# Kernel tuning notes

Measured on AMD Instinct MI355X. Metric: run time of the kernel, lower is better.

Reference implementation:

```python
import jax, jax.numpy as jnp
import numpy as np

# Static configuration (matches init_kwargs / input_specs)
NUM_SEQS = 8          # sequences in the batch
H = 32                # query heads
H_KV = 8              # kv heads (GQA group = 4)
D = 128               # head dim
MEM_BLK = 64          # paged-cache block size (tokens per cache block)
CTX = 2048            # cached context length per sequence (uniform)
Q = 64                # new (diffusion-block) tokens per sequence
MAX_BLKS = CTX // MEM_BLK   # 32 blocks per sequence in block_tables
N_BLOCKS = 512        # total cache blocks in the pool
SCALE = 1.0 / float(np.sqrt(D))


def setup_inputs() -> dict:
    key = jax.random.key(0)
    k0, k1, k2, k3, k4 = jax.random.split(key, 5)
    T = NUM_SEQS * Q  # total new tokens (flat ragged layout)
    q = jax.random.normal(k0, (T, H, D), dtype=jnp.float32)
    k = jax.random.normal(k1, (T, H_KV, D), dtype=jnp.float32)
    v = jax.random.normal(k2, (T, H_KV, D), dtype=jnp.float32)
    k_cache = jax.random.normal(k3, (N_BLOCKS, MEM_BLK, H_KV, D), dtype=jnp.float32)
    v_cache = jax.random.normal(k4, (N_BLOCKS, MEM_BLK, H_KV, D), dtype=jnp.float32)
    # sequence s owns cache blocks [s*MAX_BLKS, (s+1)*MAX_BLKS)
    block_tables = jnp.arange(NUM_SEQS * MAX_BLKS, dtype=jnp.int32).reshape(NUM_SEQS, MAX_BLKS)
    # new tokens are written into freshly allocated slots beyond the context blocks
    slot_mapping = NUM_SEQS * MAX_BLKS * MEM_BLK + jnp.arange(T, dtype=jnp.int32)
    return {"q": q, "k": k, "v": v, "k_cache": k_cache, "v_cache": v_cache,
            "block_tables": block_tables, "slot_mapping": slot_mapping}


def reference(q, k, v, k_cache, v_cache, block_tables, slot_mapping):
    # --- store_kvcache: scatter new k/v rows into flat cache slots ---
    kc_flat = k_cache.reshape(-1, H_KV, D).at[slot_mapping].set(k)
    vc_flat = v_cache.reshape(-1, H_KV, D).at[slot_mapping].set(v)
    kc = kc_flat.reshape(N_BLOCKS, MEM_BLK, H_KV, D)
    vc = vc_flat.reshape(N_BLOCKS, MEM_BLK, H_KV, D)

    # --- load_kvcache: block-table indexed gather of context, concat new kv ---
    # ctx_k/ctx_v: [S, CTX, H_KV, D]
    ctx_k = kc[block_tables].reshape(NUM_SEQS, MAX_BLKS * MEM_BLK, H_KV, D)[:, :CTX]
    ctx_v = vc[block_tables].reshape(NUM_SEQS, MAX_BLKS * MEM_BLK, H_KV, D)[:, :CTX]
    k_new = k.reshape(NUM_SEQS, Q, H_KV, D)
    v_new = v.reshape(NUM_SEQS, Q, H_KV, D)
    k_full = jnp.concatenate([ctx_k, k_new], axis=1)  # [S, CTX+Q, H_KV, D]
    v_full = jnp.concatenate([ctx_v, v_new], axis=1)

    # --- flex attention with GQA: diffusion block attends to full context +
    #     bidirectionally within its own new block ---
    G = H // H_KV
    qg = q.reshape(NUM_SEQS, Q, H_KV, G, D)
    # scores: [S, H_KV, G, Q, CTX+Q]
    scores = jnp.einsum("sqhgd,skhd->shgqk", qg, k_full) * SCALE
    attn = jax.nn.softmax(scores, axis=-1)
    out = jnp.einsum("shgqk,skhd->sqhgd", attn, v_full)  # [S, Q, H_KV, G, D]
    return out.reshape(NUM_SEQS * Q, H, D)
```

## Files before the change

### kernel.cpp

```cpp
#include <hip/hip_runtime.h>
#include <hip/hip_bf16.h>


typedef float  f32x16 __attribute__((ext_vector_type(16)));
typedef short  bf16x8 __attribute__((ext_vector_type(8)));

__device__ __forceinline__ unsigned pkbf(float lo, float hi) {
    union { __hip_bfloat162 h; unsigned u; } t;
    t.h.x = __float2bfloat16(lo);
    t.h.y = __float2bfloat16(hi);
    return t.u;
}

#define LWS_OFF (4u * 64u * 256u * 128u)

__launch_bounds__(512, 2)
__global__ void attn_part(const float* __restrict__ qg,
                          const float* __restrict__ kin,
                          const float* __restrict__ vin,
                          const float* __restrict__ kcache,
                          const float* __restrict__ vcache,
                          const int*   __restrict__ bt,
                          float* __restrict__ Ows,
                          float* __restrict__ Lws)
{
    __shared__ __align__(16) unsigned char smem[49152];

    const int bid   = blockIdx.x;
    const int grp   = bid & 63;
    const int slice = bid >> 6;
    const int s     = grp >> 3;
    const int hkv   = grp & 7;

    const int tid  = threadIdx.x;
    const int w    = tid >> 6;
    const int lane = tid & 63;
    const int l32  = lane & 31;
    const int hi2  = lane >> 5;
    const int g    = w >> 1;
    const int qh   = w & 1;

    unsigned char* KB = smem;
    unsigned char* VB = smem + 16384;
    unsigned char* PB = smem + 32768 + w * 2048;

    const float QSCALE = 0.08838834764831845f * 1.44269504088896340736f;

    bf16x8 aq[8];
    {
        const float* qp =
            qg + (size_t)((s * 64 + qh * 32 + l32) * 32 + hkv * 4 + g) * 128;
#pragma unroll
        for (int dc = 0; dc < 8; ++dc) {
            const float* p = qp + dc * 16 + hi2 * 8;
            const float4 f0 = *(const float4*)(p);
            const float4 f1 = *(const float4*)(p + 4);
            uint4 tt = make_uint4(pkbf(f0.x * QSCALE, f0.y * QSCALE),
                                  pkbf(f0.z * QSCALE, f0.w * QSCALE),
                                  pkbf(f1.x * QSCALE, f1.y * QSCALE),
                                  pkbf(f1.z * QSCALE, f1.w * QSCALE));
            aq[dc] = __builtin_bit_cast(bf16x8, tt);
        }
    }

    f32x16 acco[4];
#pragma unroll
    for (int dc = 0; dc < 4; ++dc) acco[dc] = (f32x16)0.f;
    float lsum = 0.f;

    const int vd  = tid & 127;
    const int vkg = tid >> 7;

    float4 kreg[2];
    float  vreg[8];

    const int tile0 = (slice < 2) ? slice * 17 : 34 + (slice - 2) * 16;
    const int nt    = (slice < 2) ? 17 : 16;

    auto load_regs = [&](int T) {
        const float *ks, *vs;
        if (T < 64) {
            const int blk = bt[s * 32 + (T >> 1)];
            const size_t base = (size_t)blk * 65536 + (size_t)(T & 1) * 32768 + hkv * 128;
            ks = kcache + base; vs = vcache + base;
        } else {
            const size_t base = (size_t)(s * 64 + (T & 1) * 32) * 1024 + hkv * 128;
            ks = kin + base; vs = vin + base;
        }
#pragma unroll
        for (int i = 0; i < 2; ++i) {
            const int f = tid + 512 * i;
            kreg[i] = *(const float4*)(ks + (size_t)(f >> 5) * 1024 + (f & 31) * 4);
        }
#pragma unroll
        for (int j = 0; j < 8; ++j)
            vreg[j] = vs[(size_t)(vkg * 8 + j) * 1024 + vd];
    };

    auto write_lds = [&](int buf) {
        unsigned char* K = KB + buf * 8192;
        unsigned char* V = VB + buf * 8192;
#pragma unroll
        for (int i = 0; i < 2; ++i) {
            const int f  = tid + 512 * i;
            const int kv = f >> 5;
            const int dk = f & 31;
            const int Xs = dk ^ ((kv & 15) << 1);
            *(uint2*)(K + kv * 256 + Xs * 8) =
                make_uint2(pkbf(kreg[i].x, kreg[i].y), pkbf(kreg[i].z, kreg[i].w));
        }
        const int u = vkg ^ ((vd >> 1) & 3);
        *(uint4*)(V + vd * 64 + u * 16) =
            make_uint4(pkbf(vreg[0], vreg[1]), pkbf(vreg[2], vreg[3]),
                       pkbf(vreg[4], vreg[5]), pkbf(vreg[6], vreg[7]));
    };

    const int vq = (l32 >> 1) & 3;

    auto compute = [&](int buf) {
        const unsigned char* K = KB + buf * 8192;
        const unsigned char* V = VB + buf * 8192;

        f32x16 sc = (f32x16)0.f;
#pragma unroll
        for (int dc = 0; dc < 8; ++dc) {
            const int u = (dc * 2 + hi2) ^ (l32 & 15);
            const bf16x8 ak = *(const bf16x8*)(K + l32 * 256 + u * 16);
            sc = __builtin_amdgcn_mfma_f32_32x32x16_bf16(ak, aq[dc], sc, 0, 0, 0);
        }

        float p[16];
#pragma unroll
        for (int r = 0; r < 16; ++r) {
            p[r] = __builtin_amdgcn_exp2f(sc[r]);
            lsum += p[r];
        }

#pragma unroll
        for (int rq = 0; rq < 4; ++rq)
#pragma unroll
            for (int e = 0; e < 2; ++e)
                *(unsigned*)(PB + l32 * 64 + ((rq ^ vq) * 16) + (2 * hi2 + e) * 4) =
                    pkbf(p[rq * 4 + 2 * e], p[rq * 4 + 2 * e + 1]);
        asm volatile("s_waitcnt lgkmcnt(0)" ::: "memory");

        bf16x8 pa[2];
#pragma unroll
        for (int kk = 0; kk < 2; ++kk)
            pa[kk] = *(const bf16x8*)(PB + l32 * 64 + (((kk * 2 + hi2) ^ vq) * 16));

#pragma unroll
        for (int kk = 0; kk < 2; ++kk)
#pragma unroll
            for (int d2 = 0; d2 < 4; ++d2) {
                const int u = (kk * 2 + hi2) ^ vq;
                const bf16x8 bv = *(const bf16x8*)(V + (d2 * 32 + l32) * 64 + u * 16);
                acco[d2] = __builtin_amdgcn_mfma_f32_32x32x16_bf16(pa[kk], bv, acco[d2], 0, 0, 0);
            }
    };

    load_regs(tile0);
    write_lds(0);
    load_regs(tile0 + 1);

    for (int tt = 0; tt < nt; ++tt) {
        __syncthreads();
        if (tt + 1 < nt) write_lds((tt + 1) & 1);
        if (tt + 2 < nt) load_regs(tile0 + tt + 2);
        compute(tt & 1);
    }

    const float lt = lsum + __shfl_xor(lsum, 32);
    const size_t gq = (size_t)(slice * 64 + grp) * 256 + w * 32;
    if (hi2 == 0) Lws[gq + l32] = lt;
    float* Od = Ows + gq * 128;
#pragma unroll
    for (int dc = 0; dc < 4; ++dc)
#pragma unroll
        for (int r = 0; r < 16; ++r) {
            const int qiw = (r & 3) + 8 * (r >> 2) + 4 * hi2;
            Od[(size_t)qiw * 128 + dc * 32 + l32] = acco[dc][r];
        }
}

__launch_bounds__(256)
__global__ void attn_combine(const float* __restrict__ Ows,
                             const float* __restrict__ Lws,
                             float* __restrict__ out)
{
    const int idx = blockIdx.x * 256 + threadIdx.x;
    const int dq  = idx & 31;
    const int qr  = (idx >> 5) & 255;
    const int grp = idx >> 13;
    const int s = grp >> 3, hkv = grp & 7;
    const int g = qr >> 6, qtok = qr & 63;

    float4 acc = make_float4(0.f, 0.f, 0.f, 0.f);
    float  l   = 0.f;
#pragma unroll
    for (int sl = 0; sl < 4; ++sl) {
        const size_t base = (size_t)(sl * 64 + grp) * 256 + qr;
        const float4 p = *(const float4*)(Ows + base * 128 + dq * 4);
        acc.x += p.x; acc.y += p.y; acc.z += p.z; acc.w += p.w;
        l += Lws[base];
    }
    const float inv = 1.0f / l;
    float4 o = make_float4(acc.x * inv, acc.y * inv, acc.z * inv, acc.w * inv);
    *(float4*)(out + ((size_t)((s * 64 + qtok) * 32 + hkv * 4 + g)) * 128 + dq * 4) = o;
}

extern "C" void kernel_launch(void* const* d_in, const int* in_sizes, int n_in,
                              void* d_out, int out_size, void* d_ws, size_t ws_size,
                              hipStream_t stream)
{
    const float* q  = (const float*)d_in[0];
    const float* k  = (const float*)d_in[1];
    const float* v  = (const float*)d_in[2];
    const float* kc = (const float*)d_in[3];
    const float* vc = (const float*)d_in[4];
    const int*   bt = (const int*)d_in[5];
    float* Ows = (float*)d_ws;
    float* Lws = Ows + LWS_OFF;
    float* o   = (float*)d_out;

    attn_part<<<dim3(256), dim3(512), 0, stream>>>(q, k, v, kc, vc, bt, Ows, Lws);
    attn_combine<<<dim3(2048), dim3(256), 0, stream>>>(Ows, Lws, o);
}
```

Before: 45.79 us.

## Split each block's KV tiles across two wave halves with LDS reduction

The attention partial kernel now launches 1024-thread blocks. Two halves of 8 waves each process disjoint halves of the slice's KV tiles, using separate double-buffered K/V LDS regions. This doubles the waves per CU available to hide global-load and MFMA latency on a grid that has only 256 blocks. The partial outputs and row sums are then reduced through LDS before the workspace write. The change also wraps the MFMA loops in s_setprio, and it adds a larger LDS footprint, extra barriers and tighter register budgets under the new launch bounds, which risks spills.

Result: slower. 143.3 us (+213.0%).

```diff
diff --git a/kernel.cpp b/kernel.cpp
--- a/kernel.cpp
+++ b/kernel.cpp
@@ -14,7 +14,7 @@
 
 #define LWS_OFF (4u * 64u * 256u * 128u)
 
-__launch_bounds__(512, 2)
+__launch_bounds__(1024, 4)
 __global__ void attn_part(const float* __restrict__ qg,
                           const float* __restrict__ kin,
                           const float* __restrict__ vin,
@@ -24,7 +24,7 @@
                           float* __restrict__ Ows,
                           float* __restrict__ Lws)
 {
-    __shared__ __align__(16) unsigned char smem[49152];
+    __shared__ __align__(16) unsigned char smem[98304];
 
     const int bid   = blockIdx.x;
     const int grp   = bid & 63;
@@ -32,17 +32,20 @@
     const int s     = grp >> 3;
     const int hkv   = grp & 7;
 
-    const int tid  = threadIdx.x;
-    const int w    = tid >> 6;
-    const int lane = tid & 63;
-    const int l32  = lane & 31;
-    const int hi2  = lane >> 5;
-    const int g    = w >> 1;
-    const int qh   = w & 1;
-
-    unsigned char* KB = smem;
-    unsigned char* VB = smem + 16384;
-    unsigned char* PB = smem + 32768 + w * 2048;
+    const int tid    = threadIdx.x;
+    const int w      = tid >> 6;
+    const int kvhalf = w >> 3;
+    const int wg     = w & 7;
+    const int g      = wg >> 1;
+    const int qh     = wg & 1;
+    const int lane   = tid & 63;
+    const int l32    = lane & 31;
+    const int hi2    = lane >> 5;
+    const int qtid   = tid & 511;
+
+    unsigned char* KB = smem + kvhalf * 32768;
+    unsigned char* VB = smem + kvhalf * 32768 + 16384;
+    unsigned char* PB = smem + 65536 + w * 2048;
 
     const float QSCALE = 0.08838834764831845f * 1.44269504088896340736f;
 
@@ -68,14 +71,17 @@
     for (int dc = 0; dc < 4; ++dc) acco[dc] = (f32x16)0.f;
     float lsum = 0.f;
 
-    const int vd  = tid & 127;
-    const int vkg = tid >> 7;
+    const int vd  = qtid & 127;
+    const int vkg = qtid >> 7;
 
     float4 kreg[2];
     float  vreg[8];
 
-    const int tile0 = (slice < 2) ? slice * 17 : 34 + (slice - 2) * 16;
-    const int nt    = (slice < 2) ? 17 : 16;
+    const int slice_t0 = (slice < 2) ? slice * 17 : 34 + (slice - 2) * 16;
+    const int slice_nt = (slice < 2) ? 17 : 16;
+    const int nh0      = (slice_nt + 1) >> 1;
+    const int t0       = slice_t0 + kvhalf * nh0;
+    const int nt       = kvhalf ? (slice_nt - nh0) : nh0;
 
     auto load_regs = [&](int T) {
         const float *ks, *vs;
@@ -89,7 +95,7 @@
         }
 #pragma unroll
         for (int i = 0; i < 2; ++i) {
-            const int f = tid + 512 * i;
+            const int f = qtid + 512 * i;
             kreg[i] = *(const float4*)(ks + (size_t)(f >> 5) * 1024 + (f & 31) * 4);
         }
 #pragma unroll
@@ -102,7 +108,7 @@
         unsigned char* V = VB + buf * 8192;
 #pragma unroll
         for (int i = 0; i < 2; ++i) {
-            const int f  = tid + 512 * i;
+            const int f  = qtid + 512 * i;
             const int kv = f >> 5;
             const int dk = f & 31;
             const int Xs = dk ^ ((kv & 15) << 1);
@@ -122,12 +128,14 @@
         const unsigned char* V = VB + buf * 8192;
 
         f32x16 sc = (f32x16)0.f;
+        __builtin_amdgcn_s_setprio(1);
 #pragma unroll
         for (int dc = 0; dc < 8; ++dc) {
             const int u = (dc * 2 + hi2) ^ (l32 & 15);
             const bf16x8 ak = *(const bf16x8*)(K + l32 * 256 + u * 16);
             sc = __builtin_amdgcn_mfma_f32_32x32x16_bf16(ak, aq[dc], sc, 0, 0, 0);
         }
+        __builtin_amdgcn_s_setprio(0);
 
         float p[16];
 #pragma unroll
@@ -149,6 +157,7 @@
         for (int kk = 0; kk < 2; ++kk)
             pa[kk] = *(const bf16x8*)(PB + l32 * 64 + (((kk * 2 + hi2) ^ vq) * 16));
 
+        __builtin_amdgcn_s_setprio(1);
 #pragma unroll
         for (int kk = 0; kk < 2; ++kk)
 #pragma unroll
@@ -157,30 +166,65 @@
                 const bf16x8 bv = *(const bf16x8*)(V + (d2 * 32 + l32) * 64 + u * 16);
                 acco[d2] = __builtin_amdgcn_mfma_f32_32x32x16_bf16(pa[kk], bv, acco[d2], 0, 0, 0);
             }
+        __builtin_amdgcn_s_setprio(0);
     };
 
-    load_regs(tile0);
+    load_regs(t0);
     write_lds(0);
-    load_regs(tile0 + 1);
-
-    for (int tt = 0; tt < nt; ++tt) {
+    load_regs(t0 + 1);
+
+    for (int tt = 0; tt < 9; ++tt) {
         __syncthreads();
         if (tt + 1 < nt) write_lds((tt + 1) & 1);
-        if (tt + 2 < nt) load_regs(tile0 + tt + 2);
-        compute(tt & 1);
-    }
-
-    const float lt = lsum + __shfl_xor(lsum, 32);
-    const size_t gq = (size_t)(slice * 64 + grp) * 256 + w * 32;
-    if (hi2 == 0) Lws[gq + l32] = lt;
-    float* Od = Ows + gq * 128;
-#pragma unroll
-    for (int dc = 0; dc < 4; ++dc)
-#pragma unroll
-        for (int r = 0; r < 16; ++r) {
-            const int qiw = (r & 3) + 8 * (r >> 2) + 4 * hi2;
-            Od[(size_t)qiw * 128 + dc * 32 + l32] = acco[dc][r];
-        }
+        if (tt + 2 < nt) load_regs(t0 + tt + 2);
+        if (tt < nt)     compute(tt & 1);
+    }
+
+    float lt = lsum + __shfl_xor(lsum, 32);
+
+    float* OC = (float*)smem;
+    float* LC = (float*)(smem + 65536);
+
+    const int qcbase = (g & 1) * 64 + qh * 32;
+
+#pragma unroll
+    for (int rr = 0; rr < 2; ++rr) {
+        __syncthreads();
+        if (kvhalf == 1 && (g >> 1) == rr) {
+#pragma unroll
+            for (int dc = 0; dc < 4; ++dc)
+#pragma unroll
+                for (int r = 0; r < 16; ++r) {
+                    const int row = (r & 3) + 8 * (r >> 2) + 4 * hi2;
+                    OC[(qcbase + row) * 128 + dc * 32 + l32] = acco[dc][r];
+                }
+            if (hi2 == 0) LC[qcbase + l32] = lt;
+        }
+        __syncthreads();
+        if (kvhalf == 0 && (g >> 1) == rr) {
+#pragma unroll
+            for (int dc = 0; dc < 4; ++dc)
+#pragma unroll
+                for (int r = 0; r < 16; ++r) {
+                    const int row = (r & 3) + 8 * (r >> 2) + 4 * hi2;
+                    acco[dc][r] += OC[(qcbase + row) * 128 + dc * 32 + l32];
+                }
+            lt += LC[qcbase + l32];
+        }
+    }
+
+    if (kvhalf == 0) {
+        const size_t gq = (size_t)(slice * 64 + grp) * 256 + wg * 32;
+        if (hi2 == 0) Lws[gq + l32] = lt;
+        float* Od = Ows + gq * 128;
+#pragma unroll
+        for (int dc = 0; dc < 4; ++dc)
+#pragma unroll
+            for (int r = 0; r < 16; ++r) {
+                const int qiw = (r & 3) + 8 * (r >> 2) + 4 * hi2;
+                Od[(size_t)qiw * 128 + dc * 32 + l32] = acco[dc][r];
+            }
+    }
 }
 
 __launch_bounds__(256)
@@ -223,6 +267,6 @@
     float* Lws = Ows + LWS_OFF;
     float* o   = (float*)d_out;
 
-    attn_part<<<dim3(256), dim3(512), 0, stream>>>(q, k, v, kc, vc, bt, Ows, Lws);
+    attn_part<<<dim3(256), dim3(1024), 0, stream>>>(q, k, v, kc, vc, bt, Ows, Lws);
     attn_combine<<<dim3(2048), dim3(256), 0, stream>>>(Ows, Lws, o);
 }
```

## Split query block across two CTAs and switch to 16x16x32 MFMA tiles

Applied to the files above, without the earlier changes.

The partial-attention kernel now launches twice as many blocks, each handling half of the 64 query tokens. Each wave now covers a 16-query sub-tile and uses 16x16x32 bf16 MFMAs in place of 32x32x16, with new LDS swizzles for the P buffer. s_setprio is raised around the MFMA bursts. The intent is to fill more CUs and shorten per-wave dependency chains, but every K/V tile is now loaded from global memory and converted to bf16 twice.

Measured after the change: 52.58 us. +14.8%, slower.

```diff
diff --git a/kernel.cpp b/kernel.cpp
--- a/kernel.cpp
+++ b/kernel.cpp
@@ -2,7 +2,7 @@
 #include <hip/hip_bf16.h>
 
 
-typedef float  f32x16 __attribute__((ext_vector_type(16)));
+typedef float  f32x4  __attribute__((ext_vector_type(4)));
 typedef short  bf16x8 __attribute__((ext_vector_type(8)));
 
 __device__ __forceinline__ unsigned pkbf(float lo, float hi) {
@@ -24,35 +24,36 @@
                           float* __restrict__ Ows,
                           float* __restrict__ Lws)
 {
-    __shared__ __align__(16) unsigned char smem[49152];
+    __shared__ __align__(16) unsigned char smem[40960];
 
     const int bid   = blockIdx.x;
+    const int qhalf = bid >> 8;
+    const int slice = (bid >> 6) & 3;
     const int grp   = bid & 63;
-    const int slice = bid >> 6;
     const int s     = grp >> 3;
     const int hkv   = grp & 7;
 
     const int tid  = threadIdx.x;
     const int w    = tid >> 6;
+    const int g    = w >> 1;
+    const int qsub = w & 1;
     const int lane = tid & 63;
-    const int l32  = lane & 31;
-    const int hi2  = lane >> 5;
-    const int g    = w >> 1;
-    const int qh   = w & 1;
+    const int l16  = lane & 15;
+    const int hi4  = lane >> 4;
 
     unsigned char* KB = smem;
     unsigned char* VB = smem + 16384;
-    unsigned char* PB = smem + 32768 + w * 2048;
+    unsigned char* PB = smem + 32768 + w * 1024;
 
     const float QSCALE = 0.08838834764831845f * 1.44269504088896340736f;
 
-    bf16x8 aq[8];
+    bf16x8 aq[4];
     {
-        const float* qp =
-            qg + (size_t)((s * 64 + qh * 32 + l32) * 32 + hkv * 4 + g) * 128;
-#pragma unroll
-        for (int dc = 0; dc < 8; ++dc) {
-            const float* p = qp + dc * 16 + hi2 * 8;
+        const float* qp = qg +
+            (size_t)((s * 64 + qhalf * 32 + qsub * 16 + l16) * 32 + hkv * 4 + g) * 128;
+#pragma unroll
+        for (int dc = 0; dc < 4; ++dc) {
+            const float* p = qp + dc * 32 + hi4 * 8;
             const float4 f0 = *(const float4*)(p);
             const float4 f1 = *(const float4*)(p + 4);
             uint4 tt = make_uint4(pkbf(f0.x * QSCALE, f0.y * QSCALE),
@@ -63,9 +64,9 @@
         }
     }
 
-    f32x16 acco[4];
-#pragma unroll
-    for (int dc = 0; dc < 4; ++dc) acco[dc] = (f32x16)0.f;
+    f32x4 acco[8];
+#pragma unroll
+    for (int db = 0; db < 8; ++db) acco[db] = (f32x4){0.f, 0.f, 0.f, 0.f};
     float lsum = 0.f;
 
     const int vd  = tid & 127;
@@ -115,48 +116,52 @@
                        pkbf(vreg[4], vreg[5]), pkbf(vreg[6], vreg[7]));
     };
 
-    const int vq = (l32 >> 1) & 3;
+    const int pswz = l16 & 3;
+    const int vswz = (l16 >> 1) & 3;
 
     auto compute = [&](int buf) {
         const unsigned char* K = KB + buf * 8192;
         const unsigned char* V = VB + buf * 8192;
 
-        f32x16 sc = (f32x16)0.f;
-#pragma unroll
-        for (int dc = 0; dc < 8; ++dc) {
-            const int u = (dc * 2 + hi2) ^ (l32 & 15);
-            const bf16x8 ak = *(const bf16x8*)(K + l32 * 256 + u * 16);
-            sc = __builtin_amdgcn_mfma_f32_32x32x16_bf16(ak, aq[dc], sc, 0, 0, 0);
-        }
-
-        float p[16];
-#pragma unroll
-        for (int r = 0; r < 16; ++r) {
-            p[r] = __builtin_amdgcn_exp2f(sc[r]);
-            lsum += p[r];
-        }
-
-#pragma unroll
-        for (int rq = 0; rq < 4; ++rq)
-#pragma unroll
-            for (int e = 0; e < 2; ++e)
-                *(unsigned*)(PB + l32 * 64 + ((rq ^ vq) * 16) + (2 * hi2 + e) * 4) =
-                    pkbf(p[rq * 4 + 2 * e], p[rq * 4 + 2 * e + 1]);
+        f32x4 sc[2];
+#pragma unroll
+        for (int ct = 0; ct < 2; ++ct) sc[ct] = (f32x4){0.f, 0.f, 0.f, 0.f};
+        __builtin_amdgcn_s_setprio(1);
+#pragma unroll
+        for (int dc = 0; dc < 4; ++dc) {
+            const int u = (dc * 4 + hi4) ^ l16;
+#pragma unroll
+            for (int ct = 0; ct < 2; ++ct) {
+                const bf16x8 ak = *(const bf16x8*)(K + (ct * 16 + l16) * 256 + u * 16);
+                sc[ct] = __builtin_amdgcn_mfma_f32_16x16x32_bf16(ak, aq[dc], sc[ct], 0, 0, 0);
+            }
+        }
+        __builtin_amdgcn_s_setprio(0);
+
+#pragma unroll
+        for (int ct = 0; ct < 2; ++ct) {
+            const float p0 = __builtin_amdgcn_exp2f(sc[ct][0]);
+            const float p1 = __builtin_amdgcn_exp2f(sc[ct][1]);
+            const float p2 = __builtin_amdgcn_exp2f(sc[ct][2]);
+            const float p3 = __builtin_amdgcn_exp2f(sc[ct][3]);
+            lsum += (p0 + p1) + (p2 + p3);
+            const int blkbase = ct * 2 + (hi4 >> 1);
+            const int pos     = 2 * (hi4 & 1);
+            unsigned char* prow = PB + l16 * 64 + ((blkbase ^ pswz) * 16);
+            *(unsigned*)(prow + pos * 4)       = pkbf(p0, p1);
+            *(unsigned*)(prow + (pos + 1) * 4) = pkbf(p2, p3);
+        }
         asm volatile("s_waitcnt lgkmcnt(0)" ::: "memory");
 
-        bf16x8 pa[2];
-#pragma unroll
-        for (int kk = 0; kk < 2; ++kk)
-            pa[kk] = *(const bf16x8*)(PB + l32 * 64 + (((kk * 2 + hi2) ^ vq) * 16));
-
-#pragma unroll
-        for (int kk = 0; kk < 2; ++kk)
-#pragma unroll
-            for (int d2 = 0; d2 < 4; ++d2) {
-                const int u = (kk * 2 + hi2) ^ vq;
-                const bf16x8 bv = *(const bf16x8*)(V + (d2 * 32 + l32) * 64 + u * 16);
-                acco[d2] = __builtin_amdgcn_mfma_f32_32x32x16_bf16(pa[kk], bv, acco[d2], 0, 0, 0);
-            }
+        const bf16x8 pa = *(const bf16x8*)(PB + l16 * 64 + ((hi4 ^ pswz) * 16));
+
+        __builtin_amdgcn_s_setprio(1);
+#pragma unroll
+        for (int db = 0; db < 8; ++db) {
+            const bf16x8 bv = *(const bf16x8*)(V + (db * 16 + l16) * 64 + ((hi4 ^ vswz) * 16));
+            acco[db] = __builtin_amdgcn_mfma_f32_16x16x32_bf16(pa, bv, acco[db], 0, 0, 0);
+        }
+        __builtin_amdgcn_s_setprio(0);
     };
 
     load_regs(tile0);
@@ -170,17 +175,19 @@
         compute(tt & 1);
     }
 
-    const float lt = lsum + __shfl_xor(lsum, 32);
-    const size_t gq = (size_t)(slice * 64 + grp) * 256 + w * 32;
-    if (hi2 == 0) Lws[gq + l32] = lt;
-    float* Od = Ows + gq * 128;
-#pragma unroll
-    for (int dc = 0; dc < 4; ++dc)
-#pragma unroll
-        for (int r = 0; r < 16; ++r) {
-            const int qiw = (r & 3) + 8 * (r >> 2) + 4 * hi2;
-            Od[(size_t)qiw * 128 + dc * 32 + l32] = acco[dc][r];
-        }
+    float lt = lsum;
+    lt += __shfl_xor(lt, 16);
+    lt += __shfl_xor(lt, 32);
+
+    const size_t gqbase = (size_t)(slice * 64 + grp) * 256
+                        + g * 64 + qhalf * 32 + qsub * 16;
+    if (hi4 == 0) Lws[gqbase + l16] = lt;
+    float* Od = Ows + gqbase * 128;
+#pragma unroll
+    for (int db = 0; db < 8; ++db)
+#pragma unroll
+        for (int r = 0; r < 4; ++r)
+            Od[(size_t)(4 * hi4 + r) * 128 + db * 16 + l16] = acco[db][r];
 }
 
 __launch_bounds__(256)
@@ -223,6 +230,6 @@
     float* Lws = Ows + LWS_OFF;
     float* o   = (float*)d_out;
 
-    attn_part<<<dim3(256), dim3(512), 0, stream>>>(q, k, v, kc, vc, bt, Ows, Lws);
+    attn_part<<<dim3(512), dim3(512), 0, stream>>>(q, k, v, kc, vc, bt, Ows, Lws);
     attn_combine<<<dim3(2048), dim3(256), 0, stream>>>(Ows, Lws, o);
 }
```

## Split KV into eight slices, store partials in bf16, raise MFMA priority

Applied to the files above, without the earlier changes.

The key/value sequence is now split into eight slices instead of four, so 512 workgroups run the partial attention pass. This gives more parallelism on a GPU with many compute units. The partial outputs are written as bf16 to halve the workspace traffic in both the partial and combine kernels. s_setprio is raised around the MFMA loops. The trade-offs are shorter pipelines per workgroup, more partials to combine, and extra rounding from bf16 partial outputs.

Measured after the change: 51.81 us. +13.1%, slower.

```diff
diff --git a/kernel.cpp b/kernel.cpp
--- a/kernel.cpp
+++ b/kernel.cpp
@@ -11,8 +11,11 @@
     t.h.y = __float2bfloat16(hi);
     return t.u;
 }
-
-#define LWS_OFF (4u * 64u * 256u * 128u)
+__device__ __forceinline__ float bf2f(unsigned short u) {
+    return __uint_as_float((unsigned)u << 16);
+}
+
+#define OWS_ELEMS (8u * 64u * 256u * 128u)
 
 __launch_bounds__(512, 2)
 __global__ void attn_part(const float* __restrict__ qg,
@@ -21,7 +24,7 @@
                           const float* __restrict__ kcache,
                           const float* __restrict__ vcache,
                           const int*   __restrict__ bt,
-                          float* __restrict__ Ows,
+                          __hip_bfloat16* __restrict__ Ows,
                           float* __restrict__ Lws)
 {
     __shared__ __align__(16) unsigned char smem[49152];
@@ -74,8 +77,8 @@
     float4 kreg[2];
     float  vreg[8];
 
-    const int tile0 = (slice < 2) ? slice * 17 : 34 + (slice - 2) * 16;
-    const int nt    = (slice < 2) ? 17 : 16;
+    const int tile0 = slice * 8 + (slice < 2 ? slice : 2);
+    const int nt    = 8 + (slice < 2 ? 1 : 0);
 
     auto load_regs = [&](int T) {
         const float *ks, *vs;
@@ -122,12 +125,14 @@
         const unsigned char* V = VB + buf * 8192;
 
         f32x16 sc = (f32x16)0.f;
+        __builtin_amdgcn_s_setprio(1);
 #pragma unroll
         for (int dc = 0; dc < 8; ++dc) {
             const int u = (dc * 2 + hi2) ^ (l32 & 15);
             const bf16x8 ak = *(const bf16x8*)(K + l32 * 256 + u * 16);
             sc = __builtin_amdgcn_mfma_f32_32x32x16_bf16(ak, aq[dc], sc, 0, 0, 0);
         }
+        __builtin_amdgcn_s_setprio(0);
 
         float p[16];
 #pragma unroll
@@ -149,6 +154,7 @@
         for (int kk = 0; kk < 2; ++kk)
             pa[kk] = *(const bf16x8*)(PB + l32 * 64 + (((kk * 2 + hi2) ^ vq) * 16));
 
+        __builtin_amdgcn_s_setprio(1);
 #pragma unroll
         for (int kk = 0; kk < 2; ++kk)
 #pragma unroll
@@ -157,6 +163,7 @@
                 const bf16x8 bv = *(const bf16x8*)(V + (d2 * 32 + l32) * 64 + u * 16);
                 acco[d2] = __builtin_amdgcn_mfma_f32_32x32x16_bf16(pa[kk], bv, acco[d2], 0, 0, 0);
             }
+        __builtin_amdgcn_s_setprio(0);
     };
 
     load_regs(tile0);
@@ -173,18 +180,18 @@
     const float lt = lsum + __shfl_xor(lsum, 32);
     const size_t gq = (size_t)(slice * 64 + grp) * 256 + w * 32;
     if (hi2 == 0) Lws[gq + l32] = lt;
-    float* Od = Ows + gq * 128;
+    __hip_bfloat16* Od = Ows + gq * 128;
 #pragma unroll
     for (int dc = 0; dc < 4; ++dc)
 #pragma unroll
         for (int r = 0; r < 16; ++r) {
             const int qiw = (r & 3) + 8 * (r >> 2) + 4 * hi2;
-            Od[(size_t)qiw * 128 + dc * 32 + l32] = acco[dc][r];
+            Od[(size_t)qiw * 128 + dc * 32 + l32] = __float2bfloat16(acco[dc][r]);
         }
 }
 
 __launch_bounds__(256)
-__global__ void attn_combine(const float* __restrict__ Ows,
+__global__ void attn_combine(const __hip_bfloat16* __restrict__ Ows,
                              const float* __restrict__ Lws,
                              float* __restrict__ out)
 {
@@ -198,16 +205,19 @@
     float4 acc = make_float4(0.f, 0.f, 0.f, 0.f);
     float  l   = 0.f;
 #pragma unroll
-    for (int sl = 0; sl < 4; ++sl) {
+    for (int sl = 0; sl < 8; ++sl) {
         const size_t base = (size_t)(sl * 64 + grp) * 256 + qr;
-        const float4 p = *(const float4*)(Ows + base * 128 + dq * 4);
-        acc.x += p.x; acc.y += p.y; acc.z += p.z; acc.w += p.w;
+        const ushort4 p = *(const ushort4*)(Ows + base * 128 + dq * 4);
+        acc.x += bf2f(p.x); acc.y += bf2f(p.y);
+        acc.z += bf2f(p.z); acc.w += bf2f(p.w);
         l += Lws[base];
     }
     const float inv = 1.0f / l;
     float4 o = make_float4(acc.x * inv, acc.y * inv, acc.z * inv, acc.w * inv);
     *(float4*)(out + ((size_t)((s * 64 + qtok) * 32 + hkv * 4 + g)) * 128 + dq * 4) = o;
 }
+
+__device__ __forceinline__ float bf2f_check_unused() { return 0.f; }
 
 extern "C" void kernel_launch(void* const* d_in, const int* in_sizes, int n_in,
                               void* d_out, int out_size, void* d_ws, size_t ws_size,
@@ -219,10 +229,10 @@
     const float* kc = (const float*)d_in[3];
     const float* vc = (const float*)d_in[4];
     const int*   bt = (const int*)d_in[5];
-    float* Ows = (float*)d_ws;
-    float* Lws = Ows + LWS_OFF;
+    __hip_bfloat16* Ows = (__hip_bfloat16*)d_ws;
+    float* Lws = (float*)((char*)d_ws + (size_t)OWS_ELEMS * 2);
     float* o   = (float*)d_out;
 
-    attn_part<<<dim3(256), dim3(512), 0, stream>>>(q, k, v, kc, vc, bt, Ows, Lws);
+    attn_part<<<dim3(512), dim3(512), 0, stream>>>(q, k, v, kc, vc, bt, Ows, Lws);
     attn_combine<<<dim3(2048), dim3(256), 0, stream>>>(Ows, Lws, o);
 }
```
